# Kernel optimization log

Measured on AMD Instinct MI355X. Metric: run time of the kernel, lower is better.

## Reference

```python
import jax, jax.numpy as jnp
import numpy as np

D_MODEL, D_FFN, N_LEVELS, N_HEADS, N_POINTS = 256, 1024, 4, 8, 4
B, LQ = 2, 8192
SHAPES = [(128, 128), (64, 64), (32, 32), (16, 16)]  # (H_l, W_l) per level
D_HEAD = D_MODEL // N_HEADS


def setup_inputs() -> dict:
    key = jax.random.key(0)
    ks = jax.random.split(key, 16)
    S = sum(h * w for h, w in SHAPES)

    def lin_w(k, fin, fout):
        s = 1.0 / np.sqrt(fin)
        return jax.random.uniform(k, (fin, fout), jnp.float32, -s, s)

    inp = {
        "tgt": jax.random.normal(ks[0], (B, LQ, D_MODEL), jnp.float32),
        "query_pos": jax.random.normal(ks[1], (B, LQ, D_MODEL), jnp.float32),
        "reference_points": jax.random.uniform(ks[2], (B, LQ, N_LEVELS, 2), jnp.float32),
        "src": jax.random.normal(ks[3], (B, S, D_MODEL), jnp.float32),
        "spatial_shapes": np.array(SHAPES, dtype=np.int64),
        "level_start_index": np.concatenate([[0], np.cumsum([h * w for h, w in SHAPES])[:-1]]).astype(np.int64),
        "W_value": lin_w(ks[4], D_MODEL, D_MODEL),
        "b_value": jnp.zeros((D_MODEL,), jnp.float32),
        "W_off": lin_w(ks[5], D_MODEL, N_HEADS * N_LEVELS * N_POINTS * 2),
        "b_off": 0.5 * jax.random.normal(ks[6], (N_HEADS * N_LEVELS * N_POINTS * 2,), jnp.float32),
        "W_attn": lin_w(ks[7], D_MODEL, N_HEADS * N_LEVELS * N_POINTS),
        "b_attn": jnp.zeros((N_HEADS * N_LEVELS * N_POINTS,), jnp.float32),
        "W_out": lin_w(ks[8], D_MODEL, D_MODEL),
        "b_out": jnp.zeros((D_MODEL,), jnp.float32),
        "ln1_g": jnp.ones((D_MODEL,), jnp.float32),
        "ln1_b": jnp.zeros((D_MODEL,), jnp.float32),
        "W1": lin_w(ks[9], D_MODEL, D_FFN),
        "b1": jnp.zeros((D_FFN,), jnp.float32),
        "W2": lin_w(ks[10], D_FFN, D_MODEL),
        "b2": jnp.zeros((D_MODEL,), jnp.float32),
        "ln3_g": jnp.ones((D_MODEL,), jnp.float32),
        "ln3_b": jnp.zeros((D_MODEL,), jnp.float32),
    }
    return inp


def _layer_norm(x, g, b, eps=1e-5):
    mu = jnp.mean(x, -1, keepdims=True)
    var = jnp.mean((x - mu) ** 2, -1, keepdims=True)
    return (x - mu) * jax.lax.rsqrt(var + eps) * g + b


def _ms_deform_attn(q, reference_points, src, shapes,
                    W_value, b_value, W_off, b_off, W_attn, b_attn, W_out, b_out):
    Bq, Lq, _ = q.shape
    value = (src @ W_value + b_value).reshape(Bq, -1, N_HEADS, D_HEAD)
    value = jnp.transpose(value, (0, 2, 1, 3))  # [B, H, S, Dh]
    off = (q @ W_off + b_off).reshape(Bq, Lq, N_HEADS, N_LEVELS, N_POINTS, 2)
    attn = jax.nn.softmax((q @ W_attn + b_attn).reshape(Bq, Lq, N_HEADS, N_LEVELS * N_POINTS), axis=-1)
    attn = attn.reshape(Bq, Lq, N_HEADS, N_LEVELS, N_POINTS)
    # offset normalizer is (W_l, H_l) per level
    normalizer = jnp.array([[w, h] for h, w in shapes], jnp.float32)
    loc = reference_points[:, :, None, :, None, :] + off / normalizer[None, None, None, :, None, :]

    out = jnp.zeros((Bq, Lq, N_HEADS, D_HEAD), jnp.float32)
    start = 0
    for l, (Hl, Wl) in enumerate(shapes):
        Nl = Hl * Wl
        v_l = value[:, :, start:start + Nl]  # [B, H, Nl, Dh]
        start += Nl
        loc_l = jnp.transpose(loc[:, :, :, l, :, :], (0, 2, 1, 3, 4))  # [B, H, Lq, P, 2]
        # grid_sample (align_corners=False, zero padding) pixel coords
        x = loc_l[..., 0] * Wl - 0.5
        y = loc_l[..., 1] * Hl - 0.5
        x0, y0 = jnp.floor(x), jnp.floor(y)
        wx, wy = x - x0, y - y0
        acc = jnp.zeros((Bq, N_HEADS, Lq, N_POINTS, D_HEAD), jnp.float32)
        for dx, dy, w in ((0, 0, (1 - wx) * (1 - wy)), (1, 0, wx * (1 - wy)),
                          (0, 1, (1 - wx) * wy), (1, 1, wx * wy)):
            xi, yi = x0 + dx, y0 + dy
            valid = (xi >= 0) & (xi < Wl) & (yi >= 0) & (yi < Hl)
            idx = (jnp.clip(yi, 0, Hl - 1) * Wl + jnp.clip(xi, 0, Wl - 1)).astype(jnp.int32)
            g = jnp.take_along_axis(v_l, idx.reshape(Bq, N_HEADS, -1, 1), axis=2)
            g = g.reshape(Bq, N_HEADS, Lq, N_POINTS, D_HEAD)
            acc = acc + jnp.where(valid[..., None], w[..., None] * g, 0.0)
        a = jnp.transpose(attn[:, :, :, l, :], (0, 2, 1, 3))  # [B, H, Lq, P]
        out = out + jnp.einsum('bhqp,bhqpd->bqhd', a, acc)
    return out.reshape(Bq, Lq, D_MODEL) @ W_out + b_out


def reference(tgt, query_pos, reference_points, src, spatial_shapes, level_start_index,
              W_value, b_value, W_off, b_off, W_attn, b_attn, W_out, b_out,
              ln1_g, ln1_b, W1, b1, W2, b2, ln3_g, ln3_b):
    shapes = [(int(h), int(w)) for h, w in np.asarray(spatial_shapes)]
    q = tgt + query_pos  # with_pos_embed
    tgt2 = _ms_deform_attn(q, reference_points, src, shapes,
                           W_value, b_value, W_off, b_off, W_attn, b_attn, W_out, b_out)
    x = _layer_norm(tgt + tgt2, ln1_g, ln1_b)  # dropout = identity (eval)
    ff = jax.nn.relu(x @ W1 + b1) @ W2 + b2
    return _layer_norm(x + ff, ln3_g, ln3_b)
```

## Files before the change

kernel.cpp:

```cpp
#include <hip/hip_runtime.h>
#include <hip/hip_bf16.h>
#include <hip/hip_fp16.h>
#include <math.h>

#define D_MODEL   256
#define D_FFN     1024
#define N_LEVELS  4
#define N_HEADS   8
#define N_POINTS  4
#define BATCH     2
#define LQ        8192
#define S_TOTAL   21760
#define M_Q       (BATCH*LQ)
#define M_V       (BATCH*S_TOTAL)
#define VT64      (M_V/64)

typedef __attribute__((ext_vector_type(8))) short bf16x8;
typedef __attribute__((ext_vector_type(4))) float floatx4;

struct alignas(8)  bh4 { __hip_bfloat16 a, b, c, d; };
struct alignas(16) bh8 { __hip_bfloat16 v[8]; };

__device__ __forceinline__ void gld_lds16(const void* g, void* l) {
    __builtin_amdgcn_global_load_lds(
        (const __attribute__((address_space(1))) void*)g,
        (__attribute__((address_space(3))) void*)l, 16, 0, 0);
}

__device__ __forceinline__ bh4 pack4(float4 a) {
    return { __float2bfloat16(a.x), __float2bfloat16(a.y),
             __float2bfloat16(a.z), __float2bfloat16(a.w) };
}

template<int K>
__device__ __forceinline__ void gemm_core64(const __hip_bfloat16* __restrict__ A,
                                            const __hip_bfloat16* __restrict__ Bt,
                                            int row0, int nb0, int lda, int ldb,
                                            short* As, short* Bs, floatx4 (&acc)[4])
{
    constexpr int NIT = K / 32;
    static_assert(NIT >= 2, "");
    const int tid  = threadIdx.x;
    const int w    = tid >> 6;
    const int lane = tid & 63;
    const int quad = lane >> 4;
    const int l15  = lane & 15;
    const size_t ldaB = (size_t)lda * 2, ldbB = (size_t)ldb * 2;

    const int o = w * 1024 + lane * 16;
    const char* gA = (const char*)A + (size_t)(row0 + (o >> 6)) * ldaB + (o & 63);
    const char* gB = (const char*)Bt + (size_t)(nb0 + (o >> 6)) * ldbB + (o & 63);
    const int lofs = w * 512;

    gld_lds16(gA,      As + lofs);
    gld_lds16(gB,      Bs + lofs);
    gld_lds16(gA + 64, As + 2048 + lofs);
    gld_lds16(gB + 64, Bs + 2048 + lofs);

    int oc = 0, on = 2048, of = 4096;
#pragma unroll
    for (int it = 0; it < NIT; ++it) {
        if (it + 1 < NIT) asm volatile("s_waitcnt vmcnt(2)" ::: "memory");
        else              asm volatile("s_waitcnt vmcnt(0)" ::: "memory");
        __builtin_amdgcn_s_barrier();
        __builtin_amdgcn_sched_barrier(0);
        if (it + 2 < NIT) {
            const size_t kb = (size_t)(it + 2) * 64;
            gld_lds16(gA + kb, As + of + lofs);
            gld_lds16(gB + kb, Bs + of + lofs);
        }
        const short* Ab = As + oc;
        const short* Bb = Bs + oc;
        bf16x8 af = *(const bf16x8*)&Ab[(w * 16 + l15) * 32 + quad * 8];
#pragma unroll
        for (int ni = 0; ni < 4; ni++) {
            bf16x8 bfr = *(const bf16x8*)&Bb[(ni * 16 + l15) * 32 + quad * 8];
            acc[ni] = __builtin_amdgcn_mfma_f32_16x16x32_bf16(af, bfr, acc[ni], 0, 0, 0);
        }
        int t = oc; oc = on; on = of; of = t;
    }
}

template<int K, bool ADD>
__device__ __forceinline__ void gemm_core_cvt64(const float* __restrict__ Af,
                                                const float* __restrict__ A2f,
                                                const __hip_bfloat16* __restrict__ Bt,
                                                int row0, int nb0, int lda, int ldb,
                                                short* As, short* Bs, floatx4 (&acc)[4])
{
    constexpr int NIT = K / 32;
    const int tid  = threadIdx.x;
    const int w    = tid >> 6;
    const int lane = tid & 63;
    const int quad = lane >> 4;
    const int l15  = lane & 15;

    const int o = w * 1024 + lane * 16;
    const char* gB = (const char*)Bt + (size_t)(nb0 + (o >> 6)) * ((size_t)ldb * 2) + (o & 63);
    const int lofs = w * 512;

    const int r0 = tid >> 3, k0 = (tid & 7) * 4;
    const float* gA0 = Af + (size_t)(row0 + r0) * lda + k0;
    const float* gA1 = gA0 + (size_t)32 * lda;
    const float* gB0 = ADD ? (A2f + (size_t)(row0 + r0) * lda + k0) : nullptr;
    const float* gB1 = ADD ? (gB0 + (size_t)32 * lda) : nullptr;
    const int aofs0 = r0 * 32 + k0, aofs1 = aofs0 + 1024;

    float4 f0, f1;
    auto loadA = [&](int kt) {
        f0 = *(const float4*)(gA0 + kt);
        f1 = *(const float4*)(gA1 + kt);
        if (ADD) {
            float4 a = *(const float4*)(gB0 + kt);
            float4 b = *(const float4*)(gB1 + kt);
            f0.x += a.x; f0.y += a.y; f0.z += a.z; f0.w += a.w;
            f1.x += b.x; f1.y += b.y; f1.z += b.z; f1.w += b.w;
        }
    };
    auto writeA = [&](short* buf) {
        *(bh4*)&buf[aofs0] = pack4(f0);
        *(bh4*)&buf[aofs1] = pack4(f1);
    };

    loadA(0);
    gld_lds16(gB, Bs + lofs);
    writeA(As);

#pragma unroll 8
    for (int it = 0; it < NIT; ++it) {
        __syncthreads();
        const int cb = it & 1;
        const bool more = (it + 1 < NIT);
        if (more) {
            loadA((it + 1) * 32);
            gld_lds16(gB + (size_t)(it + 1) * 64, Bs + (cb ^ 1) * 2048 + lofs);
        }
        const short* Ab = As + cb * 2048;
        const short* Bb = Bs + cb * 2048;
        bf16x8 af = *(const bf16x8*)&Ab[(w * 16 + l15) * 32 + quad * 8];
#pragma unroll
        for (int ni = 0; ni < 4; ni++) {
            bf16x8 bfr = *(const bf16x8*)&Bb[(ni * 16 + l15) * 32 + quad * 8];
            acc[ni] = __builtin_amdgcn_mfma_f32_16x16x32_bf16(af, bfr, acc[ni], 0, 0, 0);
        }
        if (more) writeA(As + (cb ^ 1) * 2048);
    }
}

template<int K, int EPI, int COLS>
__global__ __launch_bounds__(256)
void mfma_gemm64(const __hip_bfloat16* __restrict__ A,
                 const __hip_bfloat16* __restrict__ Bt,
                 const float* __restrict__ bias,
                 float* __restrict__ outf, __hip_bfloat16* __restrict__ outb,
                 int lda, int ldb, int ldOut)
{
    __shared__ alignas(16) short As[3 * 2048];
    __shared__ alignas(16) short Bs[3 * 2048];

    constexpr int BPG = 8 * COLS;
    const int g  = blockIdx.x / BPG;
    const int wq = blockIdx.x % BPG;
    const int row0 = (g * 8 + (wq & 7)) * 64;
    const int nb0  = (wq >> 3) * 64;

    const int tid = threadIdx.x, w = tid >> 6, lane = tid & 63;
    const int quad = lane >> 4, l15 = lane & 15;

    floatx4 acc[4];
#pragma unroll
    for (int ni = 0; ni < 4; ni++) acc[ni] = (floatx4){0.f, 0.f, 0.f, 0.f};

    gemm_core64<K>(A, Bt, row0, nb0, lda, ldb, As, Bs, acc);

    float bias_c[4];
#pragma unroll
    for (int ni = 0; ni < 4; ni++) bias_c[ni] = bias ? bias[nb0 + ni * 16 + l15] : 0.f;

#pragma unroll
    for (int r = 0; r < 4; r++) {
        int row = row0 + w * 16 + quad * 4 + r;
        size_t rb = (size_t)row * ldOut + nb0;
#pragma unroll
        for (int ni = 0; ni < 4; ni++) {
            float v = acc[ni][r] + bias_c[ni];
            if (EPI == 2)      outb[rb + ni * 16 + l15] = __float2bfloat16(fmaxf(v, 0.f));
            else if (EPI == 1) outb[rb + ni * 16 + l15] = __float2bfloat16(v);
            else               outf[rb + ni * 16 + l15] = v;
        }
    }
}

__global__ __launch_bounds__(256)
void mfma_gemm_vq(const float* __restrict__ src,
                  const __hip_bfloat16* __restrict__ Wvt,
                  const float* __restrict__ b_value,
                  __hip_bfloat16* __restrict__ valueb,
                  const float* __restrict__ tgt, const float* __restrict__ qpos,
                  const __hip_bfloat16* __restrict__ Woat,
                  const float* __restrict__ b_off, const float* __restrict__ b_attn,
                  float* __restrict__ offb, float* __restrict__ attnb)
{
    __shared__ alignas(16) short As[2 * 2048];
    __shared__ alignas(16) short Bs[2 * 2048];

    const int id = blockIdx.x;
    const int tid = threadIdx.x, w = tid >> 6, lane = tid & 63;
    const int quad = lane >> 4, l15 = lane & 15;

    floatx4 acc[4];
#pragma unroll
    for (int ni = 0; ni < 4; ni++) acc[ni] = (floatx4){0.f, 0.f, 0.f, 0.f};

    if (id < VT64 * 4) {
        const int g = id >> 5, wq = id & 31;
        const int row0 = (g * 8 + (wq & 7)) * 64;
        const int nb0  = (wq >> 3) * 64;
        gemm_core_cvt64<256, false>(src, nullptr, Wvt, row0, nb0, 256, 256, As, Bs, acc);
        float bias_c[4];
#pragma unroll
        for (int ni = 0; ni < 4; ni++) bias_c[ni] = b_value[nb0 + ni * 16 + l15];
#pragma unroll
        for (int r = 0; r < 4; r++) {
            int row = row0 + w * 16 + quad * 4 + r;
            size_t rb = (size_t)row * 256 + nb0;
#pragma unroll
            for (int ni = 0; ni < 4; ni++)
                valueb[rb + ni * 16 + l15] = __float2bfloat16(acc[ni][r] + bias_c[ni]);
        }
        return;
    }

    const int oid = id - VT64 * 4;
    const int g = oid / 48, wq = oid % 48;
    const int row0 = (g * 8 + (wq & 7)) * 64;
    const int c = wq >> 3;

    if (c < 4) {
        const int nb0 = c * 64;
        gemm_core_cvt64<256, true>(tgt, qpos, Woat, row0, nb0, 256, 256, As, Bs, acc);
        float bias_c[4];
#pragma unroll
        for (int ni = 0; ni < 4; ni++) bias_c[ni] = b_off[nb0 + ni * 16 + l15];
#pragma unroll
        for (int r = 0; r < 4; r++) {
            int row = row0 + w * 16 + quad * 4 + r;
            size_t rb = (size_t)row * 256 + nb0;
#pragma unroll
            for (int ni = 0; ni < 4; ni++)
                offb[rb + ni * 16 + l15] = acc[ni][r] + bias_c[ni];
        }
    } else {
        const int c0 = (c - 4) * 64;
        gemm_core_cvt64<256, true>(tgt, qpos, Woat, row0, 256 + c0, 256, 256, As, Bs, acc);
        float bias_c[4];
#pragma unroll
        for (int ni = 0; ni < 4; ni++) bias_c[ni] = b_attn[c0 + ni * 16 + l15];
#pragma unroll
        for (int r = 0; r < 4; r++) {
            int row = row0 + w * 16 + quad * 4 + r;
            size_t rb = (size_t)row * 128 + c0;
#pragma unroll
            for (int ni = 0; ni < 4; ni++) {
                float v = acc[ni][r] + bias_c[ni];
                float m = v;
#pragma unroll
                for (int msk = 1; msk <= 8; msk <<= 1) m = fmaxf(m, __shfl_xor(m, msk));
                float e = __expf(v - m);
                float ssum = e;
#pragma unroll
                for (int msk = 1; msk <= 8; msk <<= 1) ssum += __shfl_xor(ssum, msk);
                attnb[rb + ni * 16 + l15] = e / ssum;
            }
        }
    }
}

template<bool B1>
__global__ __launch_bounds__(256)
void ln_kernel(const float* __restrict__ in1f, const __hip_bfloat16* __restrict__ in1b,
               const float* __restrict__ in2,
               const float* __restrict__ resid, const float* __restrict__ bias,
               const float* __restrict__ g, const float* __restrict__ b,
               float* __restrict__ outf, __hip_bfloat16* __restrict__ outb)
{
    const int row  = blockIdx.x * 4 + (threadIdx.x >> 6);
    const int lane = threadIdx.x & 63;
    const size_t rb = (size_t)row * 256 + lane * 4;

    float4 v = *(const float4*)(resid + rb);
    if (B1) {
        bh4 a = *(const bh4*)(in1b + rb);
        v.x += __bfloat162float(a.a); v.y += __bfloat162float(a.b);
        v.z += __bfloat162float(a.c); v.w += __bfloat162float(a.d);
    } else {
        float4 a = *(const float4*)(in1f + rb);
        v.x += a.x; v.y += a.y; v.z += a.z; v.w += a.w;
    }
    if (in2) {
        float4 c = *(const float4*)(in2 + rb);
        v.x += c.x; v.y += c.y; v.z += c.z; v.w += c.w;
    }
    if (bias) {
        float4 c = *(const float4*)(bias + lane * 4);
        v.x += c.x; v.y += c.y; v.z += c.z; v.w += c.w;
    }
    float s  = v.x + v.y + v.z + v.w;
    float sq = v.x * v.x + v.y * v.y + v.z * v.z + v.w * v.w;
#pragma unroll
    for (int msk = 1; msk <= 32; msk <<= 1) {
        s += __shfl_xor(s, msk); sq += __shfl_xor(sq, msk);
    }
    float mean = s * (1.f / 256.f);
    float var  = sq * (1.f / 256.f) - mean * mean;
    float rstd = rsqrtf(var + 1e-5f);
    float4 gg = *(const float4*)(g + lane * 4);
    float4 bb = *(const float4*)(b + lane * 4);
    float4 o;
    o.x = (v.x - mean) * rstd * gg.x + bb.x;
    o.y = (v.y - mean) * rstd * gg.y + bb.y;
    o.z = (v.z - mean) * rstd * gg.z + bb.z;
    o.w = (v.w - mean) * rstd * gg.w + bb.w;
    *(float4*)(outf + rb) = o;
    if (outb)
        *(bh4*)(outb + rb) = { __float2bfloat16(o.x), __float2bfloat16(o.y),
                               __float2bfloat16(o.z), __float2bfloat16(o.w) };
}

__global__ __launch_bounds__(256)
void prep_kernel(const float* w0, const float* w1, const float* w2,
                 const float* w3, const float* w4, const float* w5,
                 __hip_bfloat16* o0, __hip_bfloat16* o1, __hip_bfloat16* o2,
                 __hip_bfloat16* o3, __hip_bfloat16* o4, __hip_bfloat16* o5)
{
    int t = blockIdx.x;
    const float* s; __hip_bfloat16* dst; int Kd, Nd, tl;
    if      (t < 64)  { s = w0; dst = o0; Kd = 256;  Nd = 256;  tl = t; }
    else if (t < 128) { s = w1; dst = o1; Kd = 256;  Nd = 256;  tl = t - 64; }
    else if (t < 160) { s = w2; dst = o2; Kd = 256;  Nd = 128;  tl = t - 128; }
    else if (t < 224) { s = w3; dst = o3; Kd = 256;  Nd = 256;  tl = t - 160; }
    else if (t < 480) { s = w4; dst = o4; Kd = 256;  Nd = 1024; tl = t - 224; }
    else              { s = w5; dst = o5; Kd = 1024; Nd = 256;  tl = t - 480; }
    int ntn = Nd >> 5;
    int kt = tl / ntn, nt = tl - kt * ntn;
    __shared__ float T[32][33];
    int tx = threadIdx.x & 31, ty = threadIdx.x >> 5;
#pragma unroll
    for (int i = 0; i < 4; i++) {
        int k = kt * 32 + ty + i * 8;
        T[tx][ty + i * 8] = s[(size_t)k * Nd + nt * 32 + tx];
    }
    __syncthreads();
#pragma unroll
    for (int i = 0; i < 4; i++) {
        int n = nt * 32 + ty + i * 8;
        dst[(size_t)n * Kd + kt * 32 + tx] = __float2bfloat16(T[ty + i * 8][tx]);
    }
}

#define QB 8
__global__ __launch_bounds__(256, 4)
void sample_kernel(const float* __restrict__ refp, const float* __restrict__ offb,
                   const float* __restrict__ attn,
                   const __hip_bfloat16* __restrict__ value,
                   __hip_bfloat16* __restrict__ tgt2)
{
    __shared__ unsigned spk[64 * 65];

    const int q0  = blockIdx.x * QB;
    const int tid = threadIdx.x;

#pragma unroll
    for (int k = 0; k < 4; k++) {
        const int it = tid + k * 256;
        const int ql = it >> 7, h = (it >> 4) & 7, lp = it & 15;
        const int l = lp >> 2, p = lp & 3;
        const int q = q0 + ql, b = q >> 13;
        const int Wl = 128 >> l;
        const int LST = (l == 0) ? 0 : (l == 1) ? 16384 : (l == 2) ? 20480 : 21504;

        const float rx = refp[((size_t)q * N_LEVELS + l) * 2 + 0];
        const float ry = refp[((size_t)q * N_LEVELS + l) * 2 + 1];
        const float ox = offb[(size_t)q * 256 + h * 32 + l * 8 + p * 2 + 0];
        const float oy = offb[(size_t)q * 256 + h * 32 + l * 8 + p * 2 + 1];
        const float a  = attn[(size_t)q * 128 + h * 16 + lp];

        const float x = rx * Wl - 0.5f + ox;
        const float y = ry * Wl - 0.5f + oy;
        const float x0f = floorf(x), y0f = floorf(y);
        const float wx = x - x0f, wy = y - y0f;
        const int ix = (int)x0f, iy = (int)y0f;
        const int base = b * S_TOTAL + LST;
        const int g = ql * 8 + h;
        const float cw[4] = {(1.f - wx) * (1.f - wy) * a, wx * (1.f - wy) * a,
                             (1.f - wx) * wy * a,         wx * wy * a};
#pragma unroll
        for (int c = 0; c < 4; c++) {
            const int xi = ix + (c & 1), yi = iy + (c >> 1);
            const bool valid = ((unsigned)xi < (unsigned)Wl) && ((unsigned)yi < (unsigned)Wl);
            const unsigned pix = valid ? (unsigned)(base + yi * Wl + xi) : (unsigned)base;
            const __half hw = __float2half(valid ? cw[c] : 0.f);
            spk[(lp * 4 + c) * 65 + g] = (pix << 16) | (unsigned)__half_as_ushort(hw);
        }
    }
    __syncthreads();

    const int ql = tid >> 5, h = (tid >> 2) & 7, d4 = tid & 3;
    const int q = q0 + ql, g = ql * 8 + h;
    const int c0 = h * 32 + d4 * 8;
    const char* vb = (const char*)value + (size_t)c0 * 2;

    float ac[8] = {0.f, 0.f, 0.f, 0.f, 0.f, 0.f, 0.f, 0.f};
#pragma unroll
    for (int ch = 0; ch < 4; ch++) {
        unsigned us[16];
#pragma unroll
        for (int j = 0; j < 16; j++) us[j] = spk[(ch * 16 + j) * 65 + g];
        uint4 rv[16];
#pragma unroll
        for (int j = 0; j < 16; j++)
            rv[j] = *(const uint4*)(vb + ((size_t)(us[j] >> 16) << 9));
#pragma unroll
        for (int j = 0; j < 16; j++) {
            float wv = __half2float(__ushort_as_half((unsigned short)(us[j] & 0xffffu)));
            ac[0] += wv * __uint_as_float(rv[j].x << 16);
            ac[1] += wv * __uint_as_float(rv[j].x & 0xffff0000u);
            ac[2] += wv * __uint_as_float(rv[j].y << 16);
            ac[3] += wv * __uint_as_float(rv[j].y & 0xffff0000u);
            ac[4] += wv * __uint_as_float(rv[j].z << 16);
            ac[5] += wv * __uint_as_float(rv[j].z & 0xffff0000u);
            ac[6] += wv * __uint_as_float(rv[j].w << 16);
            ac[7] += wv * __uint_as_float(rv[j].w & 0xffff0000u);
        }
    }
    bh8 o;
#pragma unroll
    for (int i = 0; i < 8; i++) o.v[i] = __float2bfloat16(ac[i]);
    *(bh8*)(tgt2 + (size_t)q * 256 + c0) = o;
}

extern "C" void kernel_launch(void* const* d_in, const int* in_sizes, int n_in,
                              void* d_out, int out_size, void* d_ws, size_t ws_size,
                              hipStream_t stream) {
    const float* tgt     = (const float*)d_in[0];
    const float* qpos    = (const float*)d_in[1];
    const float* refp    = (const float*)d_in[2];
    const float* src     = (const float*)d_in[3];
    const float* W_value = (const float*)d_in[6];
    const float* b_value = (const float*)d_in[7];
    const float* W_off   = (const float*)d_in[8];
    const float* b_off   = (const float*)d_in[9];
    const float* W_attn  = (const float*)d_in[10];
    const float* b_attn  = (const float*)d_in[11];
    const float* W_out   = (const float*)d_in[12];
    const float* b_out   = (const float*)d_in[13];
    const float* ln1_g   = (const float*)d_in[14];
    const float* ln1_b   = (const float*)d_in[15];
    const float* W1      = (const float*)d_in[16];
    const float* b1      = (const float*)d_in[17];
    const float* W2      = (const float*)d_in[18];
    const float* b2      = (const float*)d_in[19];
    const float* ln3_g   = (const float*)d_in[20];
    const float* ln3_b   = (const float*)d_in[21];
    float* out = (float*)d_out;

    char* p = (char*)d_ws;
    auto nxt = [&](size_t b) { char* r = p; p += (b + 255) & ~(size_t)255; return r; };
    __hip_bfloat16* Wvt    = (__hip_bfloat16*)nxt((size_t)256 * 256 * 2);
    __hip_bfloat16* Woat   = (__hip_bfloat16*)nxt((size_t)384 * 256 * 2);
    __hip_bfloat16* Woutt  = (__hip_bfloat16*)nxt((size_t)256 * 256 * 2);
    __hip_bfloat16* W1t    = (__hip_bfloat16*)nxt((size_t)1024 * 256 * 2);
    __hip_bfloat16* W2t    = (__hip_bfloat16*)nxt((size_t)256 * 1024 * 2);
    __hip_bfloat16* valueb = (__hip_bfloat16*)nxt((size_t)M_V * 256 * 2);
    float*          offb   = (float*)nxt((size_t)M_Q * 256 * 4);
    float*          attnb  = (float*)nxt((size_t)M_Q * 128 * 4);
    __hip_bfloat16* tgt2b  = (__hip_bfloat16*)nxt((size_t)M_Q * 256 * 2);
    __hip_bfloat16* t2ob   = (__hip_bfloat16*)nxt((size_t)M_Q * 256 * 2);
    float*          x      = (float*)nxt((size_t)M_Q * 256 * 4);
    __hip_bfloat16* xb     = (__hip_bfloat16*)nxt((size_t)M_Q * 256 * 2);
    __hip_bfloat16* hb     = (__hip_bfloat16*)nxt((size_t)M_Q * 1024 * 2);
    float* f2o = (float*)valueb;

    dim3 blk(256);

    prep_kernel<<<dim3(736), blk, 0, stream>>>(
        W_value, W_off, W_attn, W_out, W1, W2,
        Wvt, Woat, Woat + 256 * 256, Woutt, W1t, W2t);

    mfma_gemm_vq<<<dim3(VT64 * 4 + 256 / 8 * 48), blk, 0, stream>>>(
        src, Wvt, b_value, valueb, tgt, qpos, Woat, b_off, b_attn, offb, attnb);

    sample_kernel<<<dim3(M_Q / QB), blk, 0, stream>>>(refp, offb, attnb, valueb, tgt2b);

    mfma_gemm64<256, 1, 4><<<dim3(M_Q / 64 * 4), blk, 0, stream>>>(
        tgt2b, Woutt, b_out, nullptr, t2ob, 256, 256, 256);

    ln_kernel<true><<<dim3(M_Q / 4), blk, 0, stream>>>(
        nullptr, t2ob, nullptr, tgt, nullptr, ln1_g, ln1_b, x, xb);

    mfma_gemm64<256, 2, 16><<<dim3(M_Q / 64 * 16), blk, 0, stream>>>(
        xb, W1t, b1, nullptr, hb, 256, 256, 1024);

    mfma_gemm64<1024, 0, 4><<<dim3(M_Q / 64 * 4), blk, 0, stream>>>(
        hb, W2t, b2, f2o, nullptr, 1024, 1024, 256);

    ln_kernel<false><<<dim3(M_Q / 4), blk, 0, stream>>>(
        f2o, nullptr, nullptr, x, nullptr, ln3_g, ln3_b, out, nullptr);
}
```

Baseline: 297.4 us.

## Fuse FFN up and down projections into one kernel keeping hidden in LDS

Replaces the two separate FFN GEMM launches with one kernel. Each 512-thread block takes 32 rows, computes the ReLU hidden activations into shared memory, then runs the second GEMM from there. This removes the global write and re-read of the 16K x 1024 bf16 hidden tensor. The LN1 bf16 output is now written with an XOR-swizzled layout so the fused kernel can copy it straight into LDS without bank conflicts. The trade-off is that each block re-reads the full W1 and W2 weights from global or L2 memory, and the large LDS footprint (about 80 KB) limits occupancy.

```diff
diff --git a/kernel.cpp b/kernel.cpp
--- a/kernel.cpp
+++ b/kernel.cpp
@@ -276,6 +276,132 @@
     }
 }
 
+__global__ __launch_bounds__(512)
+void ffn_fused(const __hip_bfloat16* __restrict__ xb,
+               const __hip_bfloat16* __restrict__ W1t,
+               const float* __restrict__ b1,
+               const __hip_bfloat16* __restrict__ W2t,
+               const float* __restrict__ b2,
+               float* __restrict__ outf)
+{
+    __shared__ alignas(16) short xs[32 * 256];
+    __shared__ alignas(16) short hs[32 * 1024];
+
+    const int tid  = threadIdx.x;
+    const int w    = tid >> 6;
+    const int lane = tid & 63;
+    const int quad = lane >> 4;
+    const int l15  = lane & 15;
+    const int row0 = blockIdx.x * 32;
+
+    {
+        const char* gx = (const char*)xb + (size_t)(row0 + (tid >> 5)) * 512 + (size_t)(tid & 31) * 16;
+        char* dx = (char*)xs + (tid >> 6) * 1024;
+        gld_lds16(gx, dx);
+        gld_lds16(gx + 16 * 512, dx + 16 * 512);
+    }
+    __syncthreads();
+
+    __hip_bfloat16* hsb = (__hip_bfloat16*)hs;
+
+#pragma unroll
+    for (int ci = 0; ci < 2; ci++) {
+        const int c = w + ci * 8;
+        const char* gW = (const char*)W1t + (size_t)(c * 64 + l15) * 512 + (size_t)quad * 16;
+
+        floatx4 acc[2][4];
+#pragma unroll
+        for (int m = 0; m < 2; m++)
+#pragma unroll
+            for (int n = 0; n < 4; n++) acc[m][n] = (floatx4){0.f, 0.f, 0.f, 0.f};
+
+        bf16x8 bcur[4], bnxt[4];
+#pragma unroll
+        for (int n = 0; n < 4; n++)
+            bcur[n] = *(const bf16x8*)(gW + (size_t)n * 8192);
+
+#pragma unroll
+        for (int kk = 0; kk < 8; kk++) {
+            if (kk + 1 < 8) {
+#pragma unroll
+                for (int n = 0; n < 4; n++)
+                    bnxt[n] = *(const bf16x8*)(gW + (size_t)n * 8192 + (size_t)(kk + 1) * 64);
+            }
+            const int ac = (kk * 32 + quad * 8) ^ ((l15 & 7) << 3);
+            bf16x8 a0 = *(const bf16x8*)&xs[(0 * 16 + l15) * 256 + ac];
+            bf16x8 a1 = *(const bf16x8*)&xs[(1 * 16 + l15) * 256 + ac];
+#pragma unroll
+            for (int n = 0; n < 4; n++) {
+                acc[0][n] = __builtin_amdgcn_mfma_f32_16x16x32_bf16(a0, bcur[n], acc[0][n], 0, 0, 0);
+                acc[1][n] = __builtin_amdgcn_mfma_f32_16x16x32_bf16(a1, bcur[n], acc[1][n], 0, 0, 0);
+            }
+#pragma unroll
+            for (int n = 0; n < 4; n++) bcur[n] = bnxt[n];
+        }
+
+#pragma unroll
+        for (int n = 0; n < 4; n++) {
+            const int hc = c * 64 + n * 16 + l15;
+            const float bb = b1[hc];
+#pragma unroll
+            for (int m = 0; m < 2; m++)
+#pragma unroll
+                for (int r = 0; r < 4; r++) {
+                    const int hr = m * 16 + quad * 4 + r;
+                    hsb[hr * 1024 + (hc ^ ((hr & 7) << 3))] =
+                        __float2bfloat16(fmaxf(acc[m][n][r] + bb, 0.f));
+                }
+        }
+    }
+
+    __syncthreads();
+
+    const char* gW2 = (const char*)W2t + (size_t)(w * 32 + l15) * 2048 + (size_t)quad * 16;
+
+    floatx4 acc2[2][2];
+#pragma unroll
+    for (int m = 0; m < 2; m++)
+#pragma unroll
+        for (int n = 0; n < 2; n++) acc2[m][n] = (floatx4){0.f, 0.f, 0.f, 0.f};
+
+    bf16x8 c0[2], c1[2];
+#pragma unroll
+    for (int n = 0; n < 2; n++)
+        c0[n] = *(const bf16x8*)(gW2 + (size_t)n * 32768);
+
+#pragma unroll
+    for (int kk = 0; kk < 32; kk++) {
+        if (kk + 1 < 32) {
+#pragma unroll
+            for (int n = 0; n < 2; n++)
+                c1[n] = *(const bf16x8*)(gW2 + (size_t)n * 32768 + (size_t)(kk + 1) * 64);
+        }
+        const int ac = (kk * 32 + quad * 8) ^ ((l15 & 7) << 3);
+        bf16x8 a0 = *(const bf16x8*)&hs[(0 * 16 + l15) * 1024 + ac];
+        bf16x8 a1 = *(const bf16x8*)&hs[(1 * 16 + l15) * 1024 + ac];
+#pragma unroll
+        for (int n = 0; n < 2; n++) {
+            acc2[0][n] = __builtin_amdgcn_mfma_f32_16x16x32_bf16(a0, c0[n], acc2[0][n], 0, 0, 0);
+            acc2[1][n] = __builtin_amdgcn_mfma_f32_16x16x32_bf16(a1, c0[n], acc2[1][n], 0, 0, 0);
+        }
+#pragma unroll
+        for (int n = 0; n < 2; n++) c0[n] = c1[n];
+    }
+
+#pragma unroll
+    for (int n = 0; n < 2; n++) {
+        const int col = w * 32 + n * 16 + l15;
+        const float bb = b2[col];
+#pragma unroll
+        for (int m = 0; m < 2; m++)
+#pragma unroll
+            for (int r = 0; r < 4; r++) {
+                const int row = row0 + m * 16 + quad * 4 + r;
+                outf[(size_t)row * 256 + col] = acc2[m][n][r] + bb;
+            }
+    }
+}
+
 template<bool B1>
 __global__ __launch_bounds__(256)
 void ln_kernel(const float* __restrict__ in1f, const __hip_bfloat16* __restrict__ in1b,
@@ -322,9 +448,12 @@
     o.z = (v.z - mean) * rstd * gg.z + bb.z;
     o.w = (v.w - mean) * rstd * gg.w + bb.w;
     *(float4*)(outf + rb) = o;
-    if (outb)
-        *(bh4*)(outb + rb) = { __float2bfloat16(o.x), __float2bfloat16(o.y),
-                               __float2bfloat16(o.z), __float2bfloat16(o.w) };
+    if (outb) {
+        const int scol = (lane * 4) ^ ((row & 7) << 3);
+        *(bh4*)(outb + (size_t)row * 256 + scol) =
+            { __float2bfloat16(o.x), __float2bfloat16(o.y),
+              __float2bfloat16(o.z), __float2bfloat16(o.w) };
+    }
 }
 
 __global__ __launch_bounds__(256)
@@ -478,7 +607,6 @@
     __hip_bfloat16* t2ob   = (__hip_bfloat16*)nxt((size_t)M_Q * 256 * 2);
     float*          x      = (float*)nxt((size_t)M_Q * 256 * 4);
     __hip_bfloat16* xb     = (__hip_bfloat16*)nxt((size_t)M_Q * 256 * 2);
-    __hip_bfloat16* hb     = (__hip_bfloat16*)nxt((size_t)M_Q * 1024 * 2);
     float* f2o = (float*)valueb;
 
     dim3 blk(256);
@@ -498,11 +626,8 @@
     ln_kernel<true><<<dim3(M_Q / 4), blk, 0, stream>>>(
         nullptr, t2ob, nullptr, tgt, nullptr, ln1_g, ln1_b, x, xb);
 
-    mfma_gemm64<256, 2, 16><<<dim3(M_Q / 64 * 16), blk, 0, stream>>>(
-        xb, W1t, b1, nullptr, hb, 256, 256, 1024);
-
-    mfma_gemm64<1024, 0, 4><<<dim3(M_Q / 64 * 4), blk, 0, stream>>>(
-        hb, W2t, b2, f2o, nullptr, 1024, 1024, 256);
+    ffn_fused<<<dim3(M_Q / 32), dim3(512), 0, stream>>>(
+        xb, W1t, b1, W2t, b2, f2o);
 
     ln_kernel<false><<<dim3(M_Q / 4), blk, 0, stream>>>(
         f2o, nullptr, nullptr, x, nullptr, ln3_g, ln3_b, out, nullptr);
```

Measured after the change: 316.4 us. +6.4%, slower.
